# Optimization experiments

Measured on AMD Instinct MI355X. Metric: run time of the kernel, lower is better.

## Reference

```python
import jax, jax.numpy as jnp
import numpy as np

N, D, F, E, K = 8192, 1024, 4096, 8, 2


def setup_inputs() -> dict:
    key = jax.random.key(0)
    ks = jax.random.split(key, 4)
    x = jax.random.normal(ks[0], (N, D), dtype=jnp.float32)
    Wg = jax.random.normal(ks[1], (D, E), dtype=jnp.float32) * 0.02
    W1 = jax.random.normal(ks[2], (E, D, F), dtype=jnp.float32) * 0.02
    b1 = jnp.zeros((E, F), dtype=jnp.float32)
    W2 = jax.random.normal(ks[3], (E, F, D), dtype=jnp.float32) * 0.02
    b2 = jnp.zeros((E, D), dtype=jnp.float32)
    return {"x": x, "Wg": Wg, "W1": W1, "b1": b1, "W2": W2, "b2": b2}


def reference(x, Wg, W1, b1, W2, b2):
    # Top-k softmax gate (TopKGate): pick K experts per token, renormalize.
    logits = x @ Wg                                        # [N, E]
    probs = jax.nn.softmax(logits, axis=-1)
    gate_vals, expert_idx = jax.lax.top_k(probs, K)        # [N, K]
    gate_w = gate_vals / jnp.sum(gate_vals, axis=-1, keepdims=True)

    # Expert FFN (dispatch/combine math): the torch code sorts tokens by expert
    # id, all-to-alls them to the owning rank, applies the local Expert MLP,
    # and combines back weighted by gate_w. The jit-friendly equivalent is to
    # compute every expert's MLP for all tokens and gather the selected rows.
    h = jax.nn.relu(jnp.einsum('nd,edf->enf', x, W1) + b1[:, None, :])  # [E, N, F]
    o = jnp.einsum('enf,efd->end', h, W2) + b2[:, None, :]               # [E, N, D]

    tok = jnp.arange(x.shape[0])
    sel = o[expert_idx, tok[:, None]]                      # [N, K, D]
    y = jnp.sum(gate_w[..., None] * sel, axis=1)           # [N, D]
    return y
```

## Files before the change

### kernel.cpp

```cpp
#include <hip/hip_runtime.h>

#define N_TOK 8192
#define DIM   1024
#define FFN   4096
#define NEXP  8
#define TOPK  2
#define NENT  (N_TOK * TOPK)
#define MAXM  20

using short8  = __attribute__((ext_vector_type(8))) short;
using floatx4 = __attribute__((ext_vector_type(4))) float;

__device__ __forceinline__ unsigned short f2bf(float f) {
    union { float f; unsigned u; } v; v.f = f;
    unsigned r = v.u + 0x7fffu + ((v.u >> 16) & 1u);
    return (unsigned short)(r >> 16);
}

__device__ __forceinline__ float bf2f(unsigned short s) {
    union { unsigned u; float f; } v; v.u = ((unsigned)s) << 16;
    return v.f;
}

#define GLOAD_LDS16(gptr, lptr) __builtin_amdgcn_global_load_lds( \
    (__attribute__((address_space(1))) void*)(void*)(gptr),       \
    (__attribute__((address_space(3))) void*)(lptr), 16, 0, 0)


__global__ __launch_bounds__(256) void cvt_x_kernel(const float4* __restrict__ in,
                                                    ushort4* __restrict__ out) {
    int i = blockIdx.x * 256 + threadIdx.x;
    float4 v = in[i];
    ushort4 o;
    o.x = f2bf(v.x); o.y = f2bf(v.y); o.z = f2bf(v.z); o.w = f2bf(v.w);
    out[i] = o;
}

__global__ __launch_bounds__(256) void transpose_cvt(const float* __restrict__ in,
                                                     unsigned short* __restrict__ out,
                                                     int R, int C) {
    __shared__ float tile[64][65];
    int e  = blockIdx.z;
    int c0 = blockIdx.x * 64;
    int r0 = blockIdx.y * 64;
    const float* inp = in + (size_t)e * R * C;
    unsigned short* outp = out + (size_t)e * R * C;
    int tid = threadIdx.x;
    int lrow = tid >> 6, lcol = tid & 63;
#pragma unroll
    for (int i = 0; i < 16; i++) {
        int r = i * 4 + lrow;
        tile[r][lcol] = inp[(size_t)(r0 + r) * C + c0 + lcol];
    }
    __syncthreads();
    int r4 = (tid & 15) * 4;
#pragma unroll
    for (int i = 0; i < 4; i++) {
        int c = i * 16 + (tid >> 4);
        ushort4 o;
        o.x = f2bf(tile[r4 + 0][c]);
        o.y = f2bf(tile[r4 + 1][c]);
        o.z = f2bf(tile[r4 + 2][c]);
        o.w = f2bf(tile[r4 + 3][c]);
        *(ushort4*)&outp[(size_t)(c0 + c) * R + r0 + r4] = o;
    }
}


__global__ __launch_bounds__(256) void gating_kernel(const float* __restrict__ x,
                                                     const float* __restrict__ wg,
                                                     int* __restrict__ topk_e,
                                                     float* __restrict__ topk_w,
                                                     int* __restrict__ counts) {
    int wave = threadIdx.x >> 6, lane = threadIdx.x & 63;
    int t = blockIdx.x * 4 + wave;
    const float* xr = x + (size_t)t * DIM;
    float acc[NEXP];
#pragma unroll
    for (int e = 0; e < NEXP; e++) acc[e] = 0.f;
    for (int it = 0; it < DIM / 64; it++) {
        int d = it * 64 + lane;
        float xv = xr[d];
        const float4* wr = (const float4*)(wg + d * NEXP);
        float4 w0 = wr[0], w1 = wr[1];
        acc[0] += xv * w0.x; acc[1] += xv * w0.y; acc[2] += xv * w0.z; acc[3] += xv * w0.w;
        acc[4] += xv * w1.x; acc[5] += xv * w1.y; acc[6] += xv * w1.z; acc[7] += xv * w1.w;
    }
#pragma unroll
    for (int e = 0; e < NEXP; e++) {
#pragma unroll
        for (int off = 32; off > 0; off >>= 1) acc[e] += __shfl_xor(acc[e], off);
    }
    if (lane == 0) {
        int e1 = 0; float l1 = acc[0];
        for (int e = 1; e < NEXP; e++) if (acc[e] > l1) { l1 = acc[e]; e1 = e; }
        int e2 = -1; float l2 = -3.4e38f;
        for (int e = 0; e < NEXP; e++) if (e != e1 && acc[e] > l2) { l2 = acc[e]; e2 = e; }
        float w1v = 1.f / (1.f + expf(l2 - l1));
        topk_e[t * 2]     = e1;  topk_e[t * 2 + 1] = e2;
        topk_w[t * 2]     = w1v; topk_w[t * 2 + 1] = 1.f - w1v;
        atomicAdd(&counts[e1], 1);
        atomicAdd(&counts[e2], 1);
    }
}

__global__ void prefix_kernel(const int* __restrict__ counts, int* __restrict__ offs) {
    if (threadIdx.x == 0) {
        int s = 0;
        for (int e = 0; e < NEXP; e++) { offs[e] = s; s += counts[e]; }
        offs[NEXP] = s;
    }
}

__global__ __launch_bounds__(256) void scatter_kernel(const int* __restrict__ topk_e,
                                                      const float* __restrict__ topk_w,
                                                      const int* __restrict__ offs,
                                                      int* __restrict__ cursors,
                                                      int* __restrict__ entry_token,
                                                      int* __restrict__ entry_pos) {
    int t = blockIdx.x * 256 + threadIdx.x;
#pragma unroll
    for (int k = 0; k < TOPK; k++) {
        int e = topk_e[t * 2 + k];
        int pos = offs[e] + atomicAdd(&cursors[e], 1);
        entry_token[pos] = t;
        entry_pos[t * 2 + k] = pos;
    }
}


__global__ __launch_bounds__(256, 3) void gemm1_kernel(
    const unsigned short* __restrict__ xb,
    const unsigned short* __restrict__ w1t,
    const float* __restrict__ b1,
    const int* __restrict__ offs,
    const int* __restrict__ entry_token,
    unsigned short* __restrict__ h)
{
    int bid  = blockIdx.x;
    int e    = bid & 7;
    int grp  = bid % (8 * MAXM);
    int mt   = grp >> 3;
    int nt   = bid / (8 * MAXM);
    int base = offs[e];
    int cnt  = offs[e + 1] - base;
    int m0   = mt * 128;
    if (m0 >= cnt) return;
    int f0   = nt * 128;

    __shared__ unsigned short As[2][128 * 32];
    __shared__ unsigned short Bs[2][128 * 32];
    __shared__ int toks[128];

    int tid = threadIdx.x;
    if (tid < 128) {
        int r = m0 + tid;
        toks[tid] = entry_token[base + (r < cnt ? r : 0)];
    }
    __syncthreads();

    int wave = tid >> 6, lane = tid & 63;
    int wm = (wave >> 1) * 64, wn = (wave & 1) * 64;

    int lr = lane >> 2, sl = lane & 3;
    int g0 = (sl ^ ((lr >> 1) & 3)) * 8;
    const unsigned short* aG[2];
    const unsigned short* bG[2];
    int ldsOff[2];
#pragma unroll
    for (int c = 0; c < 2; c++) {
        int row = wave * 32 + c * 16 + lr;
        aG[c] = xb + (size_t)toks[row] * DIM + g0;
        bG[c] = w1t + ((size_t)e * FFN + f0 + row) * DIM + g0;
        ldsOff[c] = (wave * 32 + c * 16) * 32;
    }

    floatx4 acc[4][4];
#pragma unroll
    for (int i = 0; i < 4; i++)
#pragma unroll
        for (int j = 0; j < 4; j++) acc[i][j] = (floatx4)0.f;

    int quad = lane >> 4, rm = lane & 15;
    int slf  = (quad ^ ((rm >> 1) & 3)) * 8;
    int arow = (wm + rm) * 32;
    int brow = (wn + rm) * 32;

#pragma unroll
    for (int c = 0; c < 2; c++) {
        GLOAD_LDS16(aG[c], &As[0][ldsOff[c]]);
        GLOAD_LDS16(bG[c], &Bs[0][ldsOff[c]]);
        aG[c] += 32; bG[c] += 32;
    }

    int cur = 0;
    for (int kk = 0; kk < DIM / 32; kk++) {
        __syncthreads();
        short8 af[4], bfr[4];
#pragma unroll
        for (int mi = 0; mi < 4; mi++) af[mi] = *(const short8*)&As[cur][arow + mi * 512 + slf];
#pragma unroll
        for (int ni = 0; ni < 4; ni++) bfr[ni] = *(const short8*)&Bs[cur][brow + ni * 512 + slf];
        if (kk + 1 < DIM / 32) {
            int nxt = cur ^ 1;
#pragma unroll
            for (int c = 0; c < 2; c++) {
                GLOAD_LDS16(aG[c], &As[nxt][ldsOff[c]]);
                GLOAD_LDS16(bG[c], &Bs[nxt][ldsOff[c]]);
                aG[c] += 32; bG[c] += 32;
            }
        }
#pragma unroll
        for (int mi = 0; mi < 4; mi++)
#pragma unroll
            for (int ni = 0; ni < 4; ni++)
                acc[mi][ni] = __builtin_amdgcn_mfma_f32_16x16x32_bf16(af[mi], bfr[ni], acc[mi][ni], 0, 0, 0);
        cur ^= 1;
    }

#pragma unroll
    for (int mi = 0; mi < 4; mi++) {
        int mbase = wm + mi * 16 + quad * 4;
#pragma unroll
        for (int ni = 0; ni < 4; ni++) {
            int f = f0 + wn + ni * 16 + rm;
            float bias = b1[e * FFN + f];
            floatx4 v = acc[mi][ni];
#pragma unroll
            for (int r = 0; r < 4; r++) {
                int row = m0 + mbase + r;
                if (row < cnt) {
                    float t = v[r] + bias;
                    t = t > 0.f ? t : 0.f;
                    h[(size_t)(base + row) * FFN + f] = f2bf(t);
                }
            }
        }
    }
}


__global__ __launch_bounds__(256, 3) void gemm2_kernel(
    const unsigned short* __restrict__ h,
    const unsigned short* __restrict__ w2t,
    const float* __restrict__ b2,
    const int* __restrict__ offs,
    unsigned short* __restrict__ o)
{
    int bid  = blockIdx.x;
    int e    = bid & 7;
    int grp  = bid % (8 * MAXM);
    int mt   = grp >> 3;
    int nt   = bid / (8 * MAXM);
    int base = offs[e];
    int cnt  = offs[e + 1] - base;
    int m0   = mt * 128;
    if (m0 >= cnt) return;
    int n0   = nt * 128;

    __shared__ unsigned short As[2][128 * 32];
    __shared__ unsigned short Bs[2][128 * 32];

    int tid = threadIdx.x;
    int wave = tid >> 6, lane = tid & 63;
    int wm = (wave >> 1) * 64, wn = (wave & 1) * 64;

    int lr = lane >> 2, sl = lane & 3;
    int g0 = (sl ^ ((lr >> 1) & 3)) * 8;
    const unsigned short* aG[2];
    const unsigned short* bG[2];
    int ldsOff[2];
#pragma unroll
    for (int c = 0; c < 2; c++) {
        int row = wave * 32 + c * 16 + lr;
        aG[c] = h + (size_t)(base + m0 + row) * FFN + g0;
        bG[c] = w2t + ((size_t)e * DIM + n0 + row) * FFN + g0;
        ldsOff[c] = (wave * 32 + c * 16) * 32;
    }

    floatx4 acc[4][4];
#pragma unroll
    for (int i = 0; i < 4; i++)
#pragma unroll
        for (int j = 0; j < 4; j++) acc[i][j] = (floatx4)0.f;

    int quad = lane >> 4, rm = lane & 15;
    int slf  = (quad ^ ((rm >> 1) & 3)) * 8;
    int arow = (wm + rm) * 32;
    int brow = (wn + rm) * 32;

#pragma unroll
    for (int c = 0; c < 2; c++) {
        GLOAD_LDS16(aG[c], &As[0][ldsOff[c]]);
        GLOAD_LDS16(bG[c], &Bs[0][ldsOff[c]]);
        aG[c] += 32; bG[c] += 32;
    }

    int cur = 0;
    for (int kk = 0; kk < FFN / 32; kk++) {
        __syncthreads();
        short8 af[4], bfr[4];
#pragma unroll
        for (int mi = 0; mi < 4; mi++) af[mi] = *(const short8*)&As[cur][arow + mi * 512 + slf];
#pragma unroll
        for (int ni = 0; ni < 4; ni++) bfr[ni] = *(const short8*)&Bs[cur][brow + ni * 512 + slf];
        if (kk + 1 < FFN / 32) {
            int nxt = cur ^ 1;
#pragma unroll
            for (int c = 0; c < 2; c++) {
                GLOAD_LDS16(aG[c], &As[nxt][ldsOff[c]]);
                GLOAD_LDS16(bG[c], &Bs[nxt][ldsOff[c]]);
                aG[c] += 32; bG[c] += 32;
            }
        }
#pragma unroll
        for (int mi = 0; mi < 4; mi++)
#pragma unroll
            for (int ni = 0; ni < 4; ni++)
                acc[mi][ni] = __builtin_amdgcn_mfma_f32_16x16x32_bf16(af[mi], bfr[ni], acc[mi][ni], 0, 0, 0);
        cur ^= 1;
    }

#pragma unroll
    for (int mi = 0; mi < 4; mi++) {
        int mbase = wm + mi * 16 + quad * 4;
#pragma unroll
        for (int ni = 0; ni < 4; ni++) {
            int n = n0 + wn + ni * 16 + rm;
            float bias = b2[e * DIM + n];
            floatx4 v = acc[mi][ni];
#pragma unroll
            for (int r = 0; r < 4; r++) {
                int row = m0 + mbase + r;
                if (row < cnt)
                    o[(size_t)(base + row) * DIM + n] = f2bf(v[r] + bias);
            }
        }
    }
}


__global__ __launch_bounds__(256) void combine_kernel(const unsigned short* __restrict__ o,
                                                      const int* __restrict__ entry_pos,
                                                      const float* __restrict__ topk_w,
                                                      float* __restrict__ y) {
    int t = blockIdx.x;
    int d = threadIdx.x * 4;
    int p0 = entry_pos[t * 2], p1 = entry_pos[t * 2 + 1];
    float w0 = topk_w[t * 2], w1 = topk_w[t * 2 + 1];
    ushort4 a = *(const ushort4*)&o[(size_t)p0 * DIM + d];
    ushort4 b = *(const ushort4*)&o[(size_t)p1 * DIM + d];
    float4 r;
    r.x = w0 * bf2f(a.x) + w1 * bf2f(b.x);
    r.y = w0 * bf2f(a.y) + w1 * bf2f(b.y);
    r.z = w0 * bf2f(a.z) + w1 * bf2f(b.z);
    r.w = w0 * bf2f(a.w) + w1 * bf2f(b.w);
    *(float4*)&y[(size_t)t * DIM + d] = r;
}


extern "C" void kernel_launch(void* const* d_in, const int* in_sizes, int n_in,
                              void* d_out, int out_size, void* d_ws, size_t ws_size,
                              hipStream_t stream) {
    const float* x  = (const float*)d_in[0];
    const float* Wg = (const float*)d_in[1];
    const float* W1 = (const float*)d_in[2];
    const float* b1 = (const float*)d_in[3];
    const float* W2 = (const float*)d_in[4];
    const float* b2 = (const float*)d_in[5];
    float* y = (float*)d_out;

    char* p = (char*)d_ws;
    unsigned short* xb  = (unsigned short*)p; p += (size_t)N_TOK * DIM * 2;
    unsigned short* w1t = (unsigned short*)p; p += (size_t)NEXP * DIM * FFN * 2;
    unsigned short* w2t = (unsigned short*)p; p += (size_t)NEXP * DIM * FFN * 2;
    unsigned short* h   = (unsigned short*)p; p += (size_t)(NENT + 128) * FFN * 2;
    int*   topk_e      = (int*)p;   p += (size_t)N_TOK * TOPK * 4;
    float* topk_w      = (float*)p; p += (size_t)N_TOK * TOPK * 4;
    int*   entry_token = (int*)p;   p += (size_t)NENT * 4;
    int*   entry_pos   = (int*)p;   p += (size_t)NENT * 4;
    int*   counts      = (int*)p;   p += NEXP * 4;
    int*   cursors     = (int*)p;   p += NEXP * 4;
    int*   offs        = (int*)p;   p += (NEXP + 1) * 4;

    unsigned short* o = w1t;

    hipMemsetAsync(counts, 0, NEXP * 4 * 2, stream);

    cvt_x_kernel<<<(N_TOK * DIM) / (256 * 4), 256, 0, stream>>>((const float4*)x, (ushort4*)xb);
    transpose_cvt<<<dim3(FFN / 64, DIM / 64, NEXP), 256, 0, stream>>>(W1, w1t, DIM, FFN);
    transpose_cvt<<<dim3(DIM / 64, FFN / 64, NEXP), 256, 0, stream>>>(W2, w2t, FFN, DIM);
    gating_kernel<<<N_TOK / 4, 256, 0, stream>>>(x, Wg, topk_e, topk_w, counts);
    prefix_kernel<<<1, 64, 0, stream>>>(counts, offs);
    scatter_kernel<<<N_TOK / 256, 256, 0, stream>>>(topk_e, topk_w, offs, cursors, entry_token, entry_pos);
    gemm1_kernel<<<NEXP * MAXM * (FFN / 128), 256, 0, stream>>>(xb, w1t, b1, offs, entry_token, h);
    gemm2_kernel<<<NEXP * MAXM * (DIM / 128), 256, 0, stream>>>(h, w2t, b2, offs, o);
    combine_kernel<<<N_TOK, 256, 0, stream>>>(o, entry_pos, topk_w, y);
}
```

Before: 1.060 ms.

## Enlarge grouped GEMM tiles to 256 rows with 8 waves and split-K pipelining

Both expert GEMMs now use 512-thread blocks with 256-row M tiles (gemm1 also uses 256-wide N tiles). Each 64-wide K step is split into half-phases, with explicit vmcnt waits, raw s_barrier, sched barriers and setprio so global-to-LDS prefetch overlaps MFMA work. The aim is more operand reuse per LDS load and fewer barrier stalls. In exchange it uses more LDS and registers per block and pads more tail rows per expert. The padding region of h is zeroed so gemm2 reads defined data.

```diff
diff --git a/kernel.cpp b/kernel.cpp
--- a/kernel.cpp
+++ b/kernel.cpp
@@ -6,7 +6,7 @@
 #define NEXP  8
 #define TOPK  2
 #define NENT  (N_TOK * TOPK)
-#define MAXM  20
+#define MAXMT 10
 
 using short8  = __attribute__((ext_vector_type(8))) short;
 using floatx4 = __attribute__((ext_vector_type(4))) float;
@@ -25,6 +25,11 @@
 #define GLOAD_LDS16(gptr, lptr) __builtin_amdgcn_global_load_lds( \
     (__attribute__((address_space(1))) void*)(void*)(gptr),       \
     (__attribute__((address_space(3))) void*)(lptr), 16, 0, 0)
+
+#define BARRIER() asm volatile("s_barrier" ::: "memory")
+#define WAITV6()  asm volatile("s_waitcnt vmcnt(6)" ::: "memory")
+#define WAITV0()  asm volatile("s_waitcnt vmcnt(0)" ::: "memory")
+#define SCHED0()  __builtin_amdgcn_sched_barrier(0)
 
 
 __global__ __launch_bounds__(256) void cvt_x_kernel(const float4* __restrict__ in,
@@ -129,7 +134,7 @@
 }
 
 
-__global__ __launch_bounds__(256, 3) void gemm1_kernel(
+__global__ __launch_bounds__(512, 2) void gemm1_kernel(
     const unsigned short* __restrict__ xb,
     const unsigned short* __restrict__ w1t,
     const float* __restrict__ b1,
@@ -137,102 +142,156 @@
     const int* __restrict__ entry_token,
     unsigned short* __restrict__ h)
 {
+    constexpr int T = DIM / 64;
     int bid  = blockIdx.x;
     int e    = bid & 7;
-    int grp  = bid % (8 * MAXM);
-    int mt   = grp >> 3;
-    int nt   = bid / (8 * MAXM);
+    int mt   = (bid >> 3) % MAXMT;
+    int nt   = bid / (8 * MAXMT);
     int base = offs[e];
     int cnt  = offs[e + 1] - base;
-    int m0   = mt * 128;
+    int m0   = mt * 256;
     if (m0 >= cnt) return;
-    int f0   = nt * 128;
-
-    __shared__ unsigned short As[2][128 * 32];
-    __shared__ unsigned short Bs[2][128 * 32];
-    __shared__ int toks[128];
+    int f0   = nt * 256;
+
+    __shared__ unsigned short As[2 * 2 * 8192];
+    __shared__ unsigned short Bs[2 * 2 * 8192];
+    __shared__ int toks[256];
 
     int tid = threadIdx.x;
-    if (tid < 128) {
+    if (tid < 256) {
         int r = m0 + tid;
         toks[tid] = entry_token[base + (r < cnt ? r : 0)];
     }
     __syncthreads();
 
-    int wave = tid >> 6, lane = tid & 63;
-    int wm = (wave >> 1) * 64, wn = (wave & 1) * 64;
-
-    int lr = lane >> 2, sl = lane & 3;
-    int g0 = (sl ^ ((lr >> 1) & 3)) * 8;
-    const unsigned short* aG[2];
-    const unsigned short* bG[2];
-    int ldsOff[2];
-#pragma unroll
-    for (int c = 0; c < 2; c++) {
-        int row = wave * 32 + c * 16 + lr;
-        aG[c] = xb + (size_t)toks[row] * DIM + g0;
-        bG[c] = w1t + ((size_t)e * FFN + f0 + row) * DIM + g0;
-        ldsOff[c] = (wave * 32 + c * 16) * 32;
-    }
-
-    floatx4 acc[4][4];
-#pragma unroll
-    for (int i = 0; i < 4; i++)
+    int wid = tid >> 6, lane = tid & 63;
+    int wm = (wid >> 2) * 128;
+    int wn = (wid & 3) * 64;
+
+    int l4 = lane >> 2;
+    int srcoff = ((lane & 3) ^ ((lane >> 3) & 3)) * 8;
+    int r0 = wid * 16 + l4, r1 = 128 + r0;
+    const unsigned short* aS0 = xb + (size_t)toks[r0] * DIM + srcoff;
+    const unsigned short* aS1 = xb + (size_t)toks[r1] * DIM + srcoff;
+    const unsigned short* bS0 = w1t + ((size_t)e * FFN + f0 + r0) * DIM + srcoff;
+    const unsigned short* bS1 = w1t + ((size_t)e * FFN + f0 + r1) * DIM + srcoff;
+
+#define STAGE_A1(buf, kh, ko) do { \
+    GLOAD_LDS16(aS0 + (ko) + (kh) * 32, &As[(buf) * 16384 + (kh) * 8192 + wid * 512]); \
+    GLOAD_LDS16(aS1 + (ko) + (kh) * 32, &As[(buf) * 16384 + (kh) * 8192 + 4096 + wid * 512]); \
+} while (0)
+#define STAGE_B1(buf, kh, ko) do { \
+    GLOAD_LDS16(bS0 + (ko) + (kh) * 32, &Bs[(buf) * 16384 + (kh) * 8192 + wid * 512]); \
+    GLOAD_LDS16(bS1 + (ko) + (kh) * 32, &Bs[(buf) * 16384 + (kh) * 8192 + 4096 + wid * 512]); \
+} while (0)
+
+    floatx4 acc[8][4];
+#pragma unroll
+    for (int i = 0; i < 8; i++)
 #pragma unroll
         for (int j = 0; j < 4; j++) acc[i][j] = (floatx4)0.f;
 
-    int quad = lane >> 4, rm = lane & 15;
+    int rm = lane & 15, quad = lane >> 4;
     int slf  = (quad ^ ((rm >> 1) & 3)) * 8;
-    int arow = (wm + rm) * 32;
-    int brow = (wn + rm) * 32;
-
-#pragma unroll
-    for (int c = 0; c < 2; c++) {
-        GLOAD_LDS16(aG[c], &As[0][ldsOff[c]]);
-        GLOAD_LDS16(bG[c], &Bs[0][ldsOff[c]]);
-        aG[c] += 32; bG[c] += 32;
-    }
-
-    int cur = 0;
-    for (int kk = 0; kk < DIM / 32; kk++) {
-        __syncthreads();
-        short8 af[4], bfr[4];
-#pragma unroll
-        for (int mi = 0; mi < 4; mi++) af[mi] = *(const short8*)&As[cur][arow + mi * 512 + slf];
-#pragma unroll
-        for (int ni = 0; ni < 4; ni++) bfr[ni] = *(const short8*)&Bs[cur][brow + ni * 512 + slf];
-        if (kk + 1 < DIM / 32) {
-            int nxt = cur ^ 1;
-#pragma unroll
-            for (int c = 0; c < 2; c++) {
-                GLOAD_LDS16(aG[c], &As[nxt][ldsOff[c]]);
-                GLOAD_LDS16(bG[c], &Bs[nxt][ldsOff[c]]);
-                aG[c] += 32; bG[c] += 32;
-            }
-        }
-#pragma unroll
-        for (int mi = 0; mi < 4; mi++)
-#pragma unroll
-            for (int ni = 0; ni < 4; ni++)
-                acc[mi][ni] = __builtin_amdgcn_mfma_f32_16x16x32_bf16(af[mi], bfr[ni], acc[mi][ni], 0, 0, 0);
-        cur ^= 1;
-    }
-
-#pragma unroll
-    for (int mi = 0; mi < 4; mi++) {
-        int mbase = wm + mi * 16 + quad * 4;
-#pragma unroll
-        for (int ni = 0; ni < 4; ni++) {
-            int f = f0 + wn + ni * 16 + rm;
-            float bias = b1[e * FFN + f];
-            floatx4 v = acc[mi][ni];
-#pragma unroll
-            for (int r = 0; r < 4; r++) {
-                int row = m0 + mbase + r;
+    int aoff = (wm + rm) * 32 + slf;
+    int boff = (wn + rm) * 32 + slf;
+
+    STAGE_A1(0, 0, 0);
+    STAGE_B1(0, 0, 0);
+    STAGE_A1(0, 1, 0);
+    STAGE_B1(0, 1, 0);
+    STAGE_A1(1, 0, 64);
+    WAITV6();
+    BARRIER();
+
+    short8 alo[4], ahi[4], bfr[4];
+    for (int t = 0; t < T; ++t) {
+        int buf = t & 1, nxt = buf ^ 1;
+        int kN1 = ((t + 1 < T) ? (t + 1) : (T - 1)) * 64;
+        int kN2 = ((t + 2 < T) ? (t + 2) : (T - 1)) * 64;
+        const unsigned short* Ab = &As[buf * 16384];
+        const unsigned short* Bb = &Bs[buf * 16384];
+
+#pragma unroll
+        for (int i = 0; i < 4; ++i) alo[i] = *(const short8*)&Ab[aoff + i * 512];
+#pragma unroll
+        for (int i = 0; i < 4; ++i) bfr[i] = *(const short8*)&Bb[boff + i * 512];
+        STAGE_B1(nxt, 0, kN1);
+        BARRIER(); SCHED0();
+        __builtin_amdgcn_s_setprio(1);
+#pragma unroll
+        for (int i = 0; i < 4; ++i)
+#pragma unroll
+            for (int j = 0; j < 4; ++j)
+                acc[i][j] = __builtin_amdgcn_mfma_f32_16x16x32_bf16(alo[i], bfr[j], acc[i][j], 0, 0, 0);
+        __builtin_amdgcn_s_setprio(0);
+        SCHED0(); BARRIER();
+
+#pragma unroll
+        for (int i = 0; i < 4; ++i) ahi[i] = *(const short8*)&Ab[aoff + (i + 4) * 512];
+        STAGE_A1(nxt, 1, kN1);
+        WAITV6();
+        BARRIER(); SCHED0();
+        __builtin_amdgcn_s_setprio(1);
+#pragma unroll
+        for (int i = 0; i < 4; ++i)
+#pragma unroll
+            for (int j = 0; j < 4; ++j)
+                acc[i + 4][j] = __builtin_amdgcn_mfma_f32_16x16x32_bf16(ahi[i], bfr[j], acc[i + 4][j], 0, 0, 0);
+        __builtin_amdgcn_s_setprio(0);
+        SCHED0(); BARRIER();
+
+#pragma unroll
+        for (int i = 0; i < 4; ++i) alo[i] = *(const short8*)&Ab[8192 + aoff + i * 512];
+#pragma unroll
+        for (int i = 0; i < 4; ++i) bfr[i] = *(const short8*)&Bb[8192 + boff + i * 512];
+        STAGE_B1(nxt, 1, kN1);
+        BARRIER(); SCHED0();
+        __builtin_amdgcn_s_setprio(1);
+#pragma unroll
+        for (int i = 0; i < 4; ++i)
+#pragma unroll
+            for (int j = 0; j < 4; ++j)
+                acc[i][j] = __builtin_amdgcn_mfma_f32_16x16x32_bf16(alo[i], bfr[j], acc[i][j], 0, 0, 0);
+        __builtin_amdgcn_s_setprio(0);
+        SCHED0(); BARRIER();
+
+#pragma unroll
+        for (int i = 0; i < 4; ++i) ahi[i] = *(const short8*)&Ab[8192 + aoff + (i + 4) * 512];
+        STAGE_A1(buf, 0, kN2);
+        WAITV6();
+        BARRIER(); SCHED0();
+        __builtin_amdgcn_s_setprio(1);
+#pragma unroll
+        for (int i = 0; i < 4; ++i)
+#pragma unroll
+            for (int j = 0; j < 4; ++j)
+                acc[i + 4][j] = __builtin_amdgcn_mfma_f32_16x16x32_bf16(ahi[i], bfr[j], acc[i + 4][j], 0, 0, 0);
+        __builtin_amdgcn_s_setprio(0);
+        SCHED0(); BARRIER();
+    }
+    WAITV0();
+
+#undef STAGE_A1
+#undef STAGE_B1
+
+    float bs[4];
+#pragma unroll
+    for (int j = 0; j < 4; ++j) bs[j] = b1[(size_t)e * FFN + f0 + wn + j * 16 + rm];
+#pragma unroll
+    for (int i = 0; i < 8; ++i) {
+        int rb = wm + i * 16 + quad * 4;
+#pragma unroll
+        for (int j = 0; j < 4; ++j) {
+            int f = f0 + wn + j * 16 + rm;
+            floatx4 v = acc[i][j];
+#pragma unroll
+            for (int r = 0; r < 4; ++r) {
+                int row = m0 + rb + r;
                 if (row < cnt) {
-                    float t = v[r] + bias;
-                    t = t > 0.f ? t : 0.f;
-                    h[(size_t)(base + row) * FFN + f] = f2bf(t);
+                    float tv = v[r] + bs[j];
+                    tv = tv > 0.f ? tv : 0.f;
+                    h[(size_t)(base + row) * FFN + f] = f2bf(tv);
                 }
             }
         }
@@ -240,43 +299,46 @@
 }
 
 
-__global__ __launch_bounds__(256, 3) void gemm2_kernel(
+__global__ __launch_bounds__(512, 2) void gemm2_kernel(
     const unsigned short* __restrict__ h,
     const unsigned short* __restrict__ w2t,
     const float* __restrict__ b2,
     const int* __restrict__ offs,
     unsigned short* __restrict__ o)
 {
+    constexpr int T = FFN / 64;
     int bid  = blockIdx.x;
     int e    = bid & 7;
-    int grp  = bid % (8 * MAXM);
-    int mt   = grp >> 3;
-    int nt   = bid / (8 * MAXM);
+    int mt   = (bid >> 3) % MAXMT;
+    int nt   = bid / (8 * MAXMT);
     int base = offs[e];
     int cnt  = offs[e + 1] - base;
-    int m0   = mt * 128;
+    int m0   = mt * 256;
     if (m0 >= cnt) return;
     int n0   = nt * 128;
 
-    __shared__ unsigned short As[2][128 * 32];
-    __shared__ unsigned short Bs[2][128 * 32];
+    __shared__ unsigned short As[2 * 2 * 8192];
+    __shared__ unsigned short Bs[2 * 2 * 4096];
 
     int tid = threadIdx.x;
-    int wave = tid >> 6, lane = tid & 63;
-    int wm = (wave >> 1) * 64, wn = (wave & 1) * 64;
-
-    int lr = lane >> 2, sl = lane & 3;
-    int g0 = (sl ^ ((lr >> 1) & 3)) * 8;
-    const unsigned short* aG[2];
-    const unsigned short* bG[2];
-    int ldsOff[2];
-#pragma unroll
-    for (int c = 0; c < 2; c++) {
-        int row = wave * 32 + c * 16 + lr;
-        aG[c] = h + (size_t)(base + m0 + row) * FFN + g0;
-        bG[c] = w2t + ((size_t)e * DIM + n0 + row) * FFN + g0;
-        ldsOff[c] = (wave * 32 + c * 16) * 32;
-    }
+    int wid = tid >> 6, lane = tid & 63;
+    int wm = (wid >> 1) * 64;
+    int wn = (wid & 1) * 64;
+
+    int l4 = lane >> 2;
+    int srcoff = ((lane & 3) ^ ((lane >> 3) & 3)) * 8;
+    int r0 = wid * 16 + l4, r1 = 128 + r0;
+    const unsigned short* aS0 = h + (size_t)(base + m0 + r0) * FFN + srcoff;
+    const unsigned short* aS1 = h + (size_t)(base + m0 + r1) * FFN + srcoff;
+    const unsigned short* bS  = w2t + ((size_t)e * DIM + n0 + r0) * FFN + srcoff;
+
+#define STAGE_A2(buf, kh, ko) do { \
+    GLOAD_LDS16(aS0 + (ko) + (kh) * 32, &As[(buf) * 16384 + (kh) * 8192 + wid * 512]); \
+    GLOAD_LDS16(aS1 + (ko) + (kh) * 32, &As[(buf) * 16384 + (kh) * 8192 + 4096 + wid * 512]); \
+} while (0)
+#define STAGE_B2(buf, kh, ko) do { \
+    GLOAD_LDS16(bS + (ko) + (kh) * 32, &Bs[(buf) * 8192 + (kh) * 4096 + wid * 512]); \
+} while (0)
 
     floatx4 acc[4][4];
 #pragma unroll
@@ -284,56 +346,77 @@
 #pragma unroll
         for (int j = 0; j < 4; j++) acc[i][j] = (floatx4)0.f;
 
-    int quad = lane >> 4, rm = lane & 15;
+    int rm = lane & 15, quad = lane >> 4;
     int slf  = (quad ^ ((rm >> 1) & 3)) * 8;
-    int arow = (wm + rm) * 32;
-    int brow = (wn + rm) * 32;
-
-#pragma unroll
-    for (int c = 0; c < 2; c++) {
-        GLOAD_LDS16(aG[c], &As[0][ldsOff[c]]);
-        GLOAD_LDS16(bG[c], &Bs[0][ldsOff[c]]);
-        aG[c] += 32; bG[c] += 32;
-    }
-
-    int cur = 0;
-    for (int kk = 0; kk < FFN / 32; kk++) {
-        __syncthreads();
-        short8 af[4], bfr[4];
-#pragma unroll
-        for (int mi = 0; mi < 4; mi++) af[mi] = *(const short8*)&As[cur][arow + mi * 512 + slf];
-#pragma unroll
-        for (int ni = 0; ni < 4; ni++) bfr[ni] = *(const short8*)&Bs[cur][brow + ni * 512 + slf];
-        if (kk + 1 < FFN / 32) {
-            int nxt = cur ^ 1;
-#pragma unroll
-            for (int c = 0; c < 2; c++) {
-                GLOAD_LDS16(aG[c], &As[nxt][ldsOff[c]]);
-                GLOAD_LDS16(bG[c], &Bs[nxt][ldsOff[c]]);
-                aG[c] += 32; bG[c] += 32;
-            }
-        }
-#pragma unroll
-        for (int mi = 0; mi < 4; mi++)
-#pragma unroll
-            for (int ni = 0; ni < 4; ni++)
-                acc[mi][ni] = __builtin_amdgcn_mfma_f32_16x16x32_bf16(af[mi], bfr[ni], acc[mi][ni], 0, 0, 0);
-        cur ^= 1;
-    }
-
-#pragma unroll
-    for (int mi = 0; mi < 4; mi++) {
-        int mbase = wm + mi * 16 + quad * 4;
-#pragma unroll
-        for (int ni = 0; ni < 4; ni++) {
-            int n = n0 + wn + ni * 16 + rm;
-            float bias = b2[e * DIM + n];
-            floatx4 v = acc[mi][ni];
-#pragma unroll
-            for (int r = 0; r < 4; r++) {
-                int row = m0 + mbase + r;
+    int aoff = (wm + rm) * 32 + slf;
+    int boff = (wn + rm) * 32 + slf;
+
+    STAGE_A2(0, 0, 0);  STAGE_B2(0, 0, 0);
+    STAGE_A2(0, 1, 0);  STAGE_B2(0, 1, 0);
+    STAGE_A2(1, 0, 64); STAGE_B2(1, 0, 64);
+    WAITV6();
+    BARRIER();
+
+    short8 af[4], bfr[4];
+    for (int t = 0; t < T; ++t) {
+        int buf = t & 1, nxt = buf ^ 1;
+        int kN1 = ((t + 1 < T) ? (t + 1) : (T - 1)) * 64;
+        int kN2 = ((t + 2 < T) ? (t + 2) : (T - 1)) * 64;
+        const unsigned short* Ab = &As[buf * 16384];
+        const unsigned short* Bb = &Bs[buf * 8192];
+
+#pragma unroll
+        for (int i = 0; i < 4; ++i) af[i]  = *(const short8*)&Ab[aoff + i * 512];
+#pragma unroll
+        for (int i = 0; i < 4; ++i) bfr[i] = *(const short8*)&Bb[boff + i * 512];
+        STAGE_A2(nxt, 1, kN1); STAGE_B2(nxt, 1, kN1);
+        WAITV6();
+        BARRIER(); SCHED0();
+        __builtin_amdgcn_s_setprio(1);
+#pragma unroll
+        for (int i = 0; i < 4; ++i)
+#pragma unroll
+            for (int j = 0; j < 4; ++j)
+                acc[i][j] = __builtin_amdgcn_mfma_f32_16x16x32_bf16(af[i], bfr[j], acc[i][j], 0, 0, 0);
+        __builtin_amdgcn_s_setprio(0);
+        SCHED0(); BARRIER();
+
+#pragma unroll
+        for (int i = 0; i < 4; ++i) af[i]  = *(const short8*)&Ab[8192 + aoff + i * 512];
+#pragma unroll
+        for (int i = 0; i < 4; ++i) bfr[i] = *(const short8*)&Bb[4096 + boff + i * 512];
+        STAGE_A2(buf, 0, kN2); STAGE_B2(buf, 0, kN2);
+        WAITV6();
+        BARRIER(); SCHED0();
+        __builtin_amdgcn_s_setprio(1);
+#pragma unroll
+        for (int i = 0; i < 4; ++i)
+#pragma unroll
+            for (int j = 0; j < 4; ++j)
+                acc[i][j] = __builtin_amdgcn_mfma_f32_16x16x32_bf16(af[i], bfr[j], acc[i][j], 0, 0, 0);
+        __builtin_amdgcn_s_setprio(0);
+        SCHED0(); BARRIER();
+    }
+    WAITV0();
+
+#undef STAGE_A2
+#undef STAGE_B2
+
+    float bs[4];
+#pragma unroll
+    for (int j = 0; j < 4; ++j) bs[j] = b2[(size_t)e * DIM + n0 + wn + j * 16 + rm];
+#pragma unroll
+    for (int i = 0; i < 4; ++i) {
+        int rb = wm + i * 16 + quad * 4;
+#pragma unroll
+        for (int j = 0; j < 4; ++j) {
+            int n = n0 + wn + j * 16 + rm;
+            floatx4 v = acc[i][j];
+#pragma unroll
+            for (int r = 0; r < 4; ++r) {
+                int row = m0 + rb + r;
                 if (row < cnt)
-                    o[(size_t)(base + row) * DIM + n] = f2bf(v[r] + bias);
+                    o[(size_t)(base + row) * DIM + n] = f2bf(v[r] + bs[j]);
             }
         }
     }
@@ -374,7 +457,7 @@
     unsigned short* xb  = (unsigned short*)p; p += (size_t)N_TOK * DIM * 2;
     unsigned short* w1t = (unsigned short*)p; p += (size_t)NEXP * DIM * FFN * 2;
     unsigned short* w2t = (unsigned short*)p; p += (size_t)NEXP * DIM * FFN * 2;
-    unsigned short* h   = (unsigned short*)p; p += (size_t)(NENT + 128) * FFN * 2;
+    unsigned short* h   = (unsigned short*)p; p += (size_t)(NENT + 256) * FFN * 2;
     int*   topk_e      = (int*)p;   p += (size_t)N_TOK * TOPK * 4;
     float* topk_w      = (float*)p; p += (size_t)N_TOK * TOPK * 4;
     int*   entry_token = (int*)p;   p += (size_t)NENT * 4;
@@ -386,6 +469,7 @@
     unsigned short* o = w1t;
 
     hipMemsetAsync(counts, 0, NEXP * 4 * 2, stream);
+    hipMemsetAsync(h + (size_t)NENT * FFN, 0, (size_t)256 * FFN * 2, stream);
 
     cvt_x_kernel<<<(N_TOK * DIM) / (256 * 4), 256, 0, stream>>>((const float4*)x, (ushort4*)xb);
     transpose_cvt<<<dim3(FFN / 64, DIM / 64, NEXP), 256, 0, stream>>>(W1, w1t, DIM, FFN);
@@ -393,7 +477,7 @@
     gating_kernel<<<N_TOK / 4, 256, 0, stream>>>(x, Wg, topk_e, topk_w, counts);
     prefix_kernel<<<1, 64, 0, stream>>>(counts, offs);
     scatter_kernel<<<N_TOK / 256, 256, 0, stream>>>(topk_e, topk_w, offs, cursors, entry_token, entry_pos);
-    gemm1_kernel<<<NEXP * MAXM * (FFN / 128), 256, 0, stream>>>(xb, w1t, b1, offs, entry_token, h);
-    gemm2_kernel<<<NEXP * MAXM * (DIM / 128), 256, 0, stream>>>(h, w2t, b2, offs, o);
+    gemm1_kernel<<<NEXP * MAXMT * (FFN / 256), 512, 0, stream>>>(xb, w1t, b1, offs, entry_token, h);
+    gemm2_kernel<<<NEXP * MAXMT * (DIM / 128), 512, 0, stream>>>(h, w2t, b2, offs, o);
     combine_kernel<<<N_TOK, 256, 0, stream>>>(o, entry_pos, topk_w, y);
 }
```

New measurement: 1.112 ms. +4.9%, slower.

## Fuse x bf16 conversion into gating, fold prefix into scatter, remap GEMM blocks per XCD

Applied to the files above, without the earlier changes.

Removes the standalone x-to-bf16 kernel by writing bf16 x inside the gating loop, and removes the single-thread prefix kernel by having every scatter thread recompute expert offsets from counts. GEMM1/GEMM2 block indices are remapped so blocks that share an XCD (bid&7) work on the same expert and N-tile group, aiming for better L2 reuse of weight tiles. This trades two launches for scalar 2-byte stores in gating and redundant prefix sums in scatter.

```diff
diff --git a/kernel.cpp b/kernel.cpp
--- a/kernel.cpp
+++ b/kernel.cpp
@@ -26,15 +26,6 @@
     (__attribute__((address_space(1))) void*)(void*)(gptr),       \
     (__attribute__((address_space(3))) void*)(lptr), 16, 0, 0)
 
-
-__global__ __launch_bounds__(256) void cvt_x_kernel(const float4* __restrict__ in,
-                                                    ushort4* __restrict__ out) {
-    int i = blockIdx.x * 256 + threadIdx.x;
-    float4 v = in[i];
-    ushort4 o;
-    o.x = f2bf(v.x); o.y = f2bf(v.y); o.z = f2bf(v.z); o.w = f2bf(v.w);
-    out[i] = o;
-}
 
 __global__ __launch_bounds__(256) void transpose_cvt(const float* __restrict__ in,
                                                      unsigned short* __restrict__ out,
@@ -69,18 +60,21 @@
 
 __global__ __launch_bounds__(256) void gating_kernel(const float* __restrict__ x,
                                                      const float* __restrict__ wg,
+                                                     unsigned short* __restrict__ xb,
                                                      int* __restrict__ topk_e,
                                                      float* __restrict__ topk_w,
                                                      int* __restrict__ counts) {
     int wave = threadIdx.x >> 6, lane = threadIdx.x & 63;
     int t = blockIdx.x * 4 + wave;
     const float* xr = x + (size_t)t * DIM;
+    unsigned short* xbr = xb + (size_t)t * DIM;
     float acc[NEXP];
 #pragma unroll
     for (int e = 0; e < NEXP; e++) acc[e] = 0.f;
     for (int it = 0; it < DIM / 64; it++) {
         int d = it * 64 + lane;
         float xv = xr[d];
+        xbr[d] = f2bf(xv);
         const float4* wr = (const float4*)(wg + d * NEXP);
         float4 w0 = wr[0], w1 = wr[1];
         acc[0] += xv * w0.x; acc[1] += xv * w0.y; acc[2] += xv * w0.z; acc[3] += xv * w0.w;
@@ -104,25 +98,26 @@
     }
 }
 
-__global__ void prefix_kernel(const int* __restrict__ counts, int* __restrict__ offs) {
-    if (threadIdx.x == 0) {
-        int s = 0;
-        for (int e = 0; e < NEXP; e++) { offs[e] = s; s += counts[e]; }
-        offs[NEXP] = s;
-    }
-}
-
 __global__ __launch_bounds__(256) void scatter_kernel(const int* __restrict__ topk_e,
                                                       const float* __restrict__ topk_w,
-                                                      const int* __restrict__ offs,
+                                                      const int* __restrict__ counts,
+                                                      int* __restrict__ offs,
                                                       int* __restrict__ cursors,
                                                       int* __restrict__ entry_token,
                                                       int* __restrict__ entry_pos) {
+    int off_[NEXP]; int s = 0;
+#pragma unroll
+    for (int e = 0; e < NEXP; e++) { off_[e] = s; s += counts[e]; }
+    if (blockIdx.x == 0 && threadIdx.x == 0) {
+#pragma unroll
+        for (int e = 0; e < NEXP; e++) offs[e] = off_[e];
+        offs[NEXP] = s;
+    }
     int t = blockIdx.x * 256 + threadIdx.x;
 #pragma unroll
     for (int k = 0; k < TOPK; k++) {
         int e = topk_e[t * 2 + k];
-        int pos = offs[e] + atomicAdd(&cursors[e], 1);
+        int pos = off_[e] + atomicAdd(&cursors[e], 1);
         entry_token[pos] = t;
         entry_pos[t * 2 + k] = pos;
     }
@@ -137,11 +132,14 @@
     const int* __restrict__ entry_token,
     unsigned short* __restrict__ h)
 {
-    int bid  = blockIdx.x;
-    int e    = bid & 7;
-    int grp  = bid % (8 * MAXM);
-    int mt   = grp >> 3;
-    int nt   = bid / (8 * MAXM);
+    int bid   = blockIdx.x;
+    int xcd   = bid & 7;
+    int inner = bid >> 3;
+    int gq    = inner / MAXM;
+    int mt    = inner - gq * MAXM;
+    int g     = gq * 8 + xcd;
+    int e     = g >> 5;
+    int nt    = g & 31;
     int base = offs[e];
     int cnt  = offs[e + 1] - base;
     int m0   = mt * 128;
@@ -247,11 +245,14 @@
     const int* __restrict__ offs,
     unsigned short* __restrict__ o)
 {
-    int bid  = blockIdx.x;
-    int e    = bid & 7;
-    int grp  = bid % (8 * MAXM);
-    int mt   = grp >> 3;
-    int nt   = bid / (8 * MAXM);
+    int bid   = blockIdx.x;
+    int xcd   = bid & 7;
+    int inner = bid >> 3;
+    int gq    = inner / MAXM;
+    int mt    = inner - gq * MAXM;
+    int g     = gq * 8 + xcd;
+    int e     = g >> 3;
+    int nt    = g & 7;
     int base = offs[e];
     int cnt  = offs[e + 1] - base;
     int m0   = mt * 128;
@@ -387,12 +388,10 @@
 
     hipMemsetAsync(counts, 0, NEXP * 4 * 2, stream);
 
-    cvt_x_kernel<<<(N_TOK * DIM) / (256 * 4), 256, 0, stream>>>((const float4*)x, (ushort4*)xb);
     transpose_cvt<<<dim3(FFN / 64, DIM / 64, NEXP), 256, 0, stream>>>(W1, w1t, DIM, FFN);
     transpose_cvt<<<dim3(DIM / 64, FFN / 64, NEXP), 256, 0, stream>>>(W2, w2t, FFN, DIM);
-    gating_kernel<<<N_TOK / 4, 256, 0, stream>>>(x, Wg, topk_e, topk_w, counts);
-    prefix_kernel<<<1, 64, 0, stream>>>(counts, offs);
-    scatter_kernel<<<N_TOK / 256, 256, 0, stream>>>(topk_e, topk_w, offs, cursors, entry_token, entry_pos);
+    gating_kernel<<<N_TOK / 4, 256, 0, stream>>>(x, Wg, xb, topk_e, topk_w, counts);
+    scatter_kernel<<<N_TOK / 256, 256, 0, stream>>>(topk_e, topk_w, counts, offs, cursors, entry_token, entry_pos);
     gemm1_kernel<<<NEXP * MAXM * (FFN / 128), 256, 0, stream>>>(xb, w1t, b1, offs, entry_token, h);
     gemm2_kernel<<<NEXP * MAXM * (DIM / 128), 256, 0, stream>>>(h, w2t, b2, offs, o);
     combine_kernel<<<N_TOK, 256, 0, stream>>>(o, entry_pos, topk_w, y);
```

Measured after the change: 1.048 ms. No clear change (-1.2%).
